# Kernel tuning notes

Hardware: AMD Instinct MI355X
Metric: run time of the kernel (lower is better)

## Reference

```python
import jax, jax.numpy as jnp
import numpy as np

B, T, C = 2, 2048, 2048
NH, NKV = 16, 16
HD = C // NH            # 128
GATE_CH = 32
ROPE_BASE = 10000.0


def setup_inputs() -> dict:
    key = jax.random.key(0)
    ks = jax.random.split(key, 8)
    x = jax.random.normal(ks[0], (B, T, C), jnp.float32)
    ve = jax.random.normal(ks[1], (B, T, C), jnp.float32)
    # RoPE tables: half-dim rotation, shape broadcastable to [B, T, H, HD//2]
    d2 = HD // 2
    inv_freq = 1.0 / (ROPE_BASE ** (jnp.arange(d2, dtype=jnp.float32) / d2))
    angles = jnp.arange(T, dtype=jnp.float32)[:, None] * inv_freq[None, :]  # [T, d2]
    cos = jnp.cos(angles)[None, :, None, :]  # [1, T, 1, d2]
    sin = jnp.sin(angles)[None, :, None, :]
    s = 0.02
    Wq = jax.random.normal(ks[2], (C, NH * HD), jnp.float32) * s
    Wk = jax.random.normal(ks[3], (C, NKV * HD), jnp.float32) * s
    Wv = jax.random.normal(ks[4], (C, NKV * HD), jnp.float32) * s
    Wgate = jax.random.normal(ks[5], (GATE_CH, NKV), jnp.float32) * s
    Wproj = jax.random.normal(ks[6], (NH * HD, C), jnp.float32) * s
    return {"x": x, "ve": ve, "cos": cos, "sin": sin,
            "Wq": Wq, "Wk": Wk, "Wv": Wv, "Wgate": Wgate, "Wproj": Wproj}


def _apply_rotary(x, cos, sin):
    d = x.shape[3] // 2
    x1, x2 = x[..., :d], x[..., d:]
    return jnp.concatenate([x1 * cos + x2 * sin, x1 * -sin + x2 * cos], axis=3)


def _rms_norm(x):
    return x * jax.lax.rsqrt(jnp.mean(x * x, axis=-1, keepdims=True) + 1e-6)


def reference(x, ve, cos, sin, Wq, Wk, Wv, Wgate, Wproj):
    b, t, c = x.shape
    q = (x @ Wq).reshape(b, t, NH, HD)
    k = (x @ Wk).reshape(b, t, NKV, HD)
    v = (x @ Wv).reshape(b, t, NKV, HD)
    # value-embedding gate
    ve_r = ve.reshape(b, t, NKV, HD)
    gate = 2.0 * jax.nn.sigmoid(x[..., :GATE_CH] @ Wgate)  # [B, T, NKV]
    v = v + gate[..., None] * ve_r
    # RoPE then QK-RMSNorm
    q = _rms_norm(_apply_rotary(q, cos, sin))
    k = _rms_norm(_apply_rotary(k, cos, sin))
    # causal attention, scale = 1/sqrt(head_dim)
    scale = 1.0 / np.sqrt(HD).astype(np.float32)
    scores = jnp.einsum('bqhd,bkhd->bhqk', q, k) * scale
    causal = jnp.tril(jnp.ones((t, t), dtype=bool))
    scores = jnp.where(causal, scores, jnp.finfo(scores.dtype).min)
    probs = jax.nn.softmax(scores, axis=-1)
    y = jnp.einsum('bhqk,bkhd->bqhd', probs, v)
    y = y.reshape(b, t, NH * HD)
    return y @ Wproj
```

## Files before the change

### kernel.cpp

```cpp
#include <hip/hip_runtime.h>
#include <stdint.h>

typedef short bf16x8 __attribute__((ext_vector_type(8)));
typedef float f32x4 __attribute__((ext_vector_type(4)));

#define ASYNC16(g, l) __builtin_amdgcn_global_load_lds( \
    (const __attribute__((address_space(1))) unsigned int*)(g), \
    (__attribute__((address_space(3))) unsigned int*)(l), 16, 0, 0)

__device__ __forceinline__ float bf2f(short u) {
  union { unsigned int i; float f; } v;
  v.i = ((unsigned int)(unsigned short)u) << 16;
  return v.f;
}
__device__ __forceinline__ short f2bf(float f) {
  union { float f; unsigned int i; } v;
  v.f = f;
  return (short)(unsigned short)((v.i + 0x8000u) >> 16);
}
__device__ __forceinline__ float ldf(const void* p, long i, int isbf) {
  return isbf ? bf2f(((const short*)p)[i]) : ((const float*)p)[i];
}

__global__ void detect_dtype(const short* __restrict__ x, int* __restrict__ flag) {
  if (threadIdx.x == 0 && blockIdx.x == 0) {
    int cnt = 0;
    for (int i = 0; i < 128; ++i) {
      int e = (((unsigned short)x[i]) >> 7) & 0xFF;
      if (e >= 110 && e <= 136) ++cnt;
    }
    *flag = (cnt >= 120) ? 1 : 0;
  }
}

__global__ __launch_bounds__(256) void convert_x(
    const void* __restrict__ xin, short* __restrict__ xb, const int* __restrict__ flag) {
  long i = (long)blockIdx.x * 2048 + (long)threadIdx.x * 8;
  if (*flag) {
    *(bf16x8*)(xb + i) = *(const bf16x8*)((const short*)xin + i);
  } else {
    const float* xf = (const float*)xin;
    short tmp[8];
    #pragma unroll
    for (int j = 0; j < 8; ++j) tmp[j] = f2bf(xf[i + j]);
    *(bf16x8*)(xb + i) = *(bf16x8*)tmp;
  }
}

__global__ __launch_bounds__(256) void transpose_w(
    const void* __restrict__ S0, short* __restrict__ D0,
    const void* __restrict__ S1, short* __restrict__ D1,
    const void* __restrict__ S2, short* __restrict__ D2,
    const int* __restrict__ flag)
{
  int z = blockIdx.z;
  const void* S = (z == 0) ? S0 : (z == 1) ? S1 : S2;
  short* D = (z == 0) ? D0 : (z == 1) ? D1 : D2;
  int isbf = *flag;
  __shared__ short tile[32][33];
  int c0 = blockIdx.x * 32, r0 = blockIdx.y * 32;
  int tx = threadIdx.x, ty = threadIdx.y;
  #pragma unroll
  for (int i = 0; i < 4; ++i)
    tile[ty + 8*i][tx] = f2bf(ldf(S, (long)(r0 + ty + 8*i) * 2048 + c0 + tx, isbf));
  __syncthreads();
  #pragma unroll
  for (int i = 0; i < 4; ++i)
    D[(long)(c0 + ty + 8*i) * 2048 + r0 + tx] = tile[tx][ty + 8*i];
}

__global__ __launch_bounds__(256) void transpose_v(
    const short* __restrict__ Vr, short* __restrict__ Vt)
{
  __shared__ short tile[32][33];
  int bh = blockIdx.z;
  int b = bh >> 4, h = bh & 15;
  int t0 = blockIdx.x * 32, d0 = blockIdx.y * 32;
  int tx = threadIdx.x, ty = threadIdx.y;
  #pragma unroll
  for (int i = 0; i < 4; ++i)
    tile[ty + 8*i][tx] = Vr[(long)(b*2048 + t0 + ty + 8*i) * 2048 + h*128 + d0 + tx];
  __syncthreads();
  #pragma unroll
  for (int i = 0; i < 4; ++i)
    Vt[((long)bh * 128 + d0 + ty + 8*i) * 2048 + t0 + tx] = tile[tx][ty + 8*i];
}

template<typename OutT>
__global__ __launch_bounds__(256) void gemm_bt(
    const short* __restrict__ A,
    const short* __restrict__ B0, const short* __restrict__ B1, const short* __restrict__ B2,
    OutT* __restrict__ C0, OutT* __restrict__ C1, OutT* __restrict__ C2,
    int M, int N, int K)
{
  int z = blockIdx.z;
  const short* Bt = (z == 0) ? B0 : (z == 1) ? B1 : B2;
  OutT* C = (z == 0) ? C0 : (z == 1) ? C1 : C2;

  int d = blockIdx.y * 16 + blockIdx.x;
  int xcd = d & 7, ci = d >> 3;
  int bx = (xcd & 1) * 8 + (ci & 7);
  int by = (xcd >> 1) * 8 + (ci >> 3);
  int m0 = by * 128, n0 = bx * 128;

  int tid = threadIdx.x;
  int lane = tid & 63, w = tid >> 6;
  int quad = lane >> 4, l16 = lane & 15;
  int wm = w >> 1, wn = w & 1;

  __shared__ short As[128][64];
  __shared__ short Bs[128][64];

  f32x4 zero4 = {0.f, 0.f, 0.f, 0.f};
  f32x4 acc[4][4];
  #pragma unroll
  for (int i = 0; i < 4; ++i)
    #pragma unroll
    for (int j = 0; j < 4; ++j) acc[i][j] = zero4;

  int r8 = lane >> 3;
  int srow = w * 32 + r8;
  int scol = ((lane & 7) ^ r8) * 8;

  for (int k0 = 0; k0 < K; k0 += 64) {
    #pragma unroll
    for (int i = 0; i < 4; ++i) {
      ASYNC16(A  + (long)(m0 + srow + i*8) * K + k0 + scol, &As[w*32 + i*8][0]);
      ASYNC16(Bt + (long)(n0 + srow + i*8) * K + k0 + scol, &Bs[w*32 + i*8][0]);
    }
    __syncthreads();
    #pragma unroll
    for (int kt = 0; kt < 2; ++kt) {
      int po = ((kt*4 + quad) ^ (l16 & 7)) * 8;
      bf16x8 af[4], bfr[4];
      #pragma unroll
      for (int i = 0; i < 4; ++i)
        af[i] = *(const bf16x8*)&As[wm*64 + i*16 + l16][po];
      #pragma unroll
      for (int j = 0; j < 4; ++j)
        bfr[j] = *(const bf16x8*)&Bs[wn*64 + j*16 + l16][po];
      #pragma unroll
      for (int i = 0; i < 4; ++i)
        #pragma unroll
        for (int j = 0; j < 4; ++j)
          acc[i][j] = __builtin_amdgcn_mfma_f32_16x16x32_bf16(af[i], bfr[j], acc[i][j], 0, 0, 0);
    }
    __syncthreads();
  }

  #pragma unroll
  for (int i = 0; i < 4; ++i)
    #pragma unroll
    for (int j = 0; j < 4; ++j) {
      int row = m0 + wm*64 + i*16 + quad*4;
      int col = n0 + wn*64 + j*16 + l16;
      #pragma unroll
      for (int r = 0; r < 4; ++r) {
        float v = acc[i][j][r];
        if constexpr (sizeof(OutT) == 4)
          C[(long)(row + r) * N + col] = v;
        else
          C[(long)(row + r) * N + col] = (OutT)f2bf(v);
      }
    }
}

__global__ __launch_bounds__(256) void pointwise(
    const short* __restrict__ xb, const void* __restrict__ ve,
    const void* __restrict__ cosb, const void* __restrict__ sinb,
    const void* __restrict__ Wg, const int* __restrict__ flag,
    short* __restrict__ Qr, short* __restrict__ Kr, short* __restrict__ Vr)
{
  int row = blockIdx.x;
  int tid = threadIdx.x;
  int isbf = *flag;
  __shared__ float xg[32];
  __shared__ float gates[16];
  if (tid < 32) xg[tid] = bf2f(xb[(long)row * 2048 + tid]);
  __syncthreads();
  if (tid < 16) {
    float g = 0.f;
    #pragma unroll
    for (int i = 0; i < 32; ++i) g += xg[i] * ldf(Wg, i*16 + tid, isbf);
    gates[tid] = 2.0f / (1.0f + __expf(-g));
  }
  __syncthreads();
  {
    int idx = tid * 8;
    int h = idx >> 7;
    long p = (long)row * 2048 + idx;
    float g = gates[h];
    bf16x8 vv = *(bf16x8*)(Vr + p);
    short tmp[8];
    if (isbf) {
      bf16x8 vb = *(const bf16x8*)((const short*)ve + p);
      #pragma unroll
      for (int j = 0; j < 8; ++j) tmp[j] = f2bf(bf2f(vv[j]) + g * bf2f(vb[j]));
    } else {
      const float* vf = (const float*)ve;
      f32x4 a = *(const f32x4*)(vf + p);
      f32x4 b2 = *(const f32x4*)(vf + p + 4);
      #pragma unroll
      for (int j = 0; j < 4; ++j) tmp[j]     = f2bf(bf2f(vv[j])     + g * a[j]);
      #pragma unroll
      for (int j = 0; j < 4; ++j) tmp[j + 4] = f2bf(bf2f(vv[j + 4]) + g * b2[j]);
    }
    *(bf16x8*)(Vr + p) = *(bf16x8*)tmp;
  }
  int lane = tid & 63, w = tid >> 6;
  int t = row & 2047;
  #pragma unroll
  for (int it = 0; it < 8; ++it) {
    int unit = it * 4 + w;
    short* P = (unit < 16) ? Qr : Kr;
    int h = unit & 15;
    long base = (long)row * 2048 + h * 128;
    float x1 = bf2f(P[base + lane]);
    float x2 = bf2f(P[base + lane + 64]);
    float c = ldf(cosb, t*64 + lane, isbf);
    float s = ldf(sinb, t*64 + lane, isbf);
    float r1 = x1 * c + x2 * s;
    float r2 = -x1 * s + x2 * c;
    float ss = r1*r1 + r2*r2;
    #pragma unroll
    for (int off = 32; off; off >>= 1) ss += __shfl_xor(ss, off);
    float rn = rsqrtf(ss * (1.0f/128.0f) + 1e-6f);
    P[base + lane]      = f2bf(r1 * rn);
    P[base + lane + 64] = f2bf(r2 * rn);
  }
}

#define FL_C1 0.12751741f
#define FL_C2 16.321698f

__global__ __launch_bounds__(256) void flash(
    const short* __restrict__ Q, const short* __restrict__ K,
    const short* __restrict__ Vt, short* __restrict__ Y)
{
  int d = blockIdx.y * 16 + blockIdx.x;
  int xcd = d & 7, ci = d >> 3;
  int bx = ci & 15;
  int bh = xcd * 4 + (ci >> 4);
  int b = bh >> 4, h = bh & 15;
  int tid = threadIdx.x;
  int lane = tid & 63, w = tid >> 6;
  int quad = lane >> 4, l16 = lane & 15;

  __shared__ short Ks[2][64*128];
  __shared__ short Vts[2][128*64];
  __shared__ short Ps[4][16*72];

  int qtA = bx, qtB = 31 - bx;
  int nA = qtA + 1, nB = qtB + 1;
  int total = nA + nB;

  int kkey = tid >> 4;
  int klo  = (tid & 15) ^ (kkey & 7);
  int vd   = tid >> 3;
  int vlo  = (tid & 7) ^ (vd & 7);
  const short* Kbase = K + (long)(b*2048 + kkey) * 2048 + h*128 + klo*8;
  const short* Vbase = Vt + ((long)bh*128 + vd) * 2048 + vlo*8;

  f32x4 zero4 = {0.f, 0.f, 0.f, 0.f};
  f32x4 o[8];
  float l_i[4];
  bf16x8 qf[4];
  bf16x8 ones;
  #pragma unroll
  for (int j = 0; j < 8; ++j) ones[j] = (short)0x3F80;

  auto stage = [&](int tt, int bufp) {
    int tl = (tt < nA) ? tt : tt - nA;
    long ko = (long)tl * 64 * 2048;
    int  vo = tl * 64;
    #pragma unroll
    for (int i = 0; i < 4; ++i)
      ASYNC16(Kbase + ko + (long)i*16*2048, &Ks[bufp][(i*16 + w*4)*128]);
    #pragma unroll
    for (int i = 0; i < 4; ++i)
      ASYNC16(Vbase + vo + (long)i*32*2048, &Vts[bufp][(i*32 + w*8)*64]);
  };
  auto loadQ = [&](int qt) {
    const short* Qb = Q + (long)(b*2048 + qt*64 + w*16 + l16) * 2048 + h*128;
    #pragma unroll
    for (int kt = 0; kt < 4; ++kt)
      qf[kt] = *(const bf16x8*)(Qb + kt*32 + quad*8);
  };
  auto flushO = [&](int qt) {
    #pragma unroll
    for (int r = 0; r < 4; ++r) {
      float inv = 1.0f / fmaxf(l_i[r], 1e-30f);
      short* yp = Y + (long)(b*2048 + qt*64 + w*16 + quad*4 + r) * 2048 + h*128;
      #pragma unroll
      for (int c8 = 0; c8 < 8; ++c8)
        yp[c8*16 + l16] = f2bf(o[c8][r] * inv);
    }
  };

  #pragma unroll
  for (int c = 0; c < 8; ++c) o[c] = zero4;
  #pragma unroll
  for (int r = 0; r < 4; ++r) l_i[r] = 0.f;
  loadQ(qtA);
  stage(0, 0);

  int qt = qtA, n_seg = nA, segbase = 0;
  for (int tt = 0; tt < total; ++tt) {
    int buf = tt & 1;
    asm volatile("s_waitcnt vmcnt(0)" ::: "memory");
    __builtin_amdgcn_s_barrier();
    if (tt + 1 < total) stage(tt + 1, buf ^ 1);
    if (tt == nA) {
      flushO(qtA);
      loadQ(qtB);
      #pragma unroll
      for (int c = 0; c < 8; ++c) o[c] = zero4;
      #pragma unroll
      for (int r = 0; r < 4; ++r) l_i[r] = 0.f;
      qt = qtB; n_seg = nB; segbase = nA;
    }
    int tloc = tt - segbase;
    int kv0 = tloc * 64;

    f32x4 s[4];
    __builtin_amdgcn_s_setprio(1);
    #pragma unroll
    for (int c = 0; c < 4; ++c) {
      f32x4 acc = zero4;
      #pragma unroll
      for (int kt = 0; kt < 4; ++kt) {
        int po = ((kt*4 + quad) ^ (l16 & 7)) * 8;
        bf16x8 kf = *(const bf16x8*)&Ks[buf][(c*16 + l16)*128 + po];
        acc = __builtin_amdgcn_mfma_f32_16x16x32_bf16(qf[kt], kf, acc, 0, 0, 0);
      }
      s[c] = acc;
    }
    __builtin_amdgcn_s_setprio(0);

    bool domask = (tloc == n_seg - 1);
    int qgb = qt*64 + w*16 + quad*4;
    #pragma unroll
    for (int c = 0; c < 4; ++c) {
      int kg = kv0 + c*16 + l16;
      #pragma unroll
      for (int r = 0; r < 4; ++r) {
        float t = s[c][r] * FL_C1 - FL_C2;
        if (domask && kg > qgb + r) t = -1000.0f;
        float pv = exp2f(t);
        Ps[w][(quad*4 + r)*72 + c*16 + l16] = f2bf(pv);
      }
    }
    asm volatile("s_waitcnt lgkmcnt(0)" ::: "memory");
    bf16x8 pa0 = *(const bf16x8*)&Ps[w][l16*72 + quad*8];
    bf16x8 pa1 = *(const bf16x8*)&Ps[w][l16*72 + 32 + quad*8];

    __builtin_amdgcn_s_setprio(1);
    f32x4 racc = __builtin_amdgcn_mfma_f32_16x16x32_bf16(pa0, ones, zero4, 0, 0, 0);
    racc = __builtin_amdgcn_mfma_f32_16x16x32_bf16(pa1, ones, racc, 0, 0, 0);
    #pragma unroll
    for (int r = 0; r < 4; ++r) l_i[r] += racc[r];

    #pragma unroll
    for (int c8 = 0; c8 < 8; ++c8) {
      int po0 = ((0*4 + quad) ^ (l16 & 7)) * 8;
      int po1 = ((1*4 + quad) ^ (l16 & 7)) * 8;
      bf16x8 v0 = *(const bf16x8*)&Vts[buf][(c8*16 + l16)*64 + po0];
      bf16x8 v1 = *(const bf16x8*)&Vts[buf][(c8*16 + l16)*64 + po1];
      o[c8] = __builtin_amdgcn_mfma_f32_16x16x32_bf16(pa0, v0, o[c8], 0, 0, 0);
      o[c8] = __builtin_amdgcn_mfma_f32_16x16x32_bf16(pa1, v1, o[c8], 0, 0, 0);
    }
    __builtin_amdgcn_s_setprio(0);
  }
  flushO(qtB);
}

extern "C" void kernel_launch(void* const* d_in, const int* in_sizes, int n_in,
                              void* d_out, int out_size, void* d_ws, size_t ws_size,
                              hipStream_t stream) {
  const void* x    = d_in[0];
  const void* ve   = d_in[1];
  const void* cosb = d_in[2];
  const void* sinb = d_in[3];
  const void* Wq   = d_in[4];
  const void* Wk   = d_in[5];
  const void* Wv   = d_in[6];
  const void* Wg   = d_in[7];
  const void* Wp   = d_in[8];
  float* out = (float*)d_out;

  int*   flag = (int*)d_ws;
  short* base = (short*)d_ws + 256;
  short* wt0 = base;
  short* wtk = base + 4194304L;
  short* wtv = base + 8388608L;
  short* Vt  = base + 4194304L;
  short* xb  = base + 12582912L;
  short* Y   = base + 12582912L;
  short* Qr  = base + 20971520L;
  short* Kr  = base + 29360128L;
  short* Vr  = base + 37748736L;

  detect_dtype<<<1, 64, 0, stream>>>((const short*)x, flag);
  convert_x<<<4096, 256, 0, stream>>>(x, xb, flag);
  transpose_w<<<dim3(64, 64, 3), dim3(32, 8), 0, stream>>>(Wq, wt0, Wk, wtk, Wv, wtv, flag);
  gemm_bt<short><<<dim3(16, 32, 3), 256, 0, stream>>>(xb, wt0, wtk, wtv, Qr, Kr, Vr, 4096, 2048, 2048);
  transpose_w<<<dim3(64, 64, 1), dim3(32, 8), 0, stream>>>(Wp, wt0, Wp, wt0, Wp, wt0, flag);
  pointwise<<<dim3(4096), 256, 0, stream>>>(xb, ve, cosb, sinb, Wg, flag, Qr, Kr, Vr);
  transpose_v<<<dim3(64, 4, 32), dim3(32, 8), 0, stream>>>(Vr, Vt);
  flash<<<dim3(16, 32), 256, 0, stream>>>(Qr, Kr, Vt, Y);
  gemm_bt<float><<<dim3(16, 32, 1), 256, 0, stream>>>(Y, wt0, wt0, wt0, out, out, out, 4096, 2048, 2048);
}
```

Before: 456.7 us.

## Share K/V tiles between paired query tiles in flash attention loop

The flash kernel used to walk the two paired query tiles (qtA and 31-qtA) one after the other, loading every K/V tile for each. Now it keeps two sets of Q fragments and accumulators and does one pass over the KV tiles of the longer segment. Each staged K/V tile is applied to both query tiles while it is still in range, which roughly halves global-to-LDS traffic. Launch bounds now ask for 2 blocks per CU, and the doubled accumulator state raises register pressure, so spills or lower occupancy are a risk.

```diff
diff --git a/kernel.cpp b/kernel.cpp
--- a/kernel.cpp
+++ b/kernel.cpp
@@ -233,7 +233,7 @@
 #define FL_C1 0.12751741f
 #define FL_C2 16.321698f
 
-__global__ __launch_bounds__(256) void flash(
+__global__ __launch_bounds__(256, 2) void flash(
     const short* __restrict__ Q, const short* __restrict__ K,
     const short* __restrict__ Vt, short* __restrict__ Y)
 {
@@ -252,7 +252,6 @@
 
   int qtA = bx, qtB = 31 - bx;
   int nA = qtA + 1, nB = qtB + 1;
-  int total = nA + nB;
 
   int kkey = tid >> 4;
   int klo  = (tid & 15) ^ (kkey & 7);
@@ -262,15 +261,17 @@
   const short* Vbase = Vt + ((long)bh*128 + vd) * 2048 + vlo*8;
 
   f32x4 zero4 = {0.f, 0.f, 0.f, 0.f};
-  f32x4 o[8];
-  float l_i[4];
-  bf16x8 qf[4];
+  f32x4 oA[8], oB[8];
+  float lA[4], lB[4];
+  bf16x8 qfA[4], qfB[4];
   bf16x8 ones;
   #pragma unroll
   for (int j = 0; j < 8; ++j) ones[j] = (short)0x3F80;
 
-  auto stage = [&](int tt, int bufp) {
-    int tl = (tt < nA) ? tt : tt - nA;
+  int pv0 = ((0*4 + quad) ^ (l16 & 7)) * 8;
+  int pv1 = ((1*4 + quad) ^ (l16 & 7)) * 8;
+
+  auto stage = [&](int tl, int bufp) {
     long ko = (long)tl * 64 * 2048;
     int  vo = tl * 64;
     #pragma unroll
@@ -280,48 +281,24 @@
     for (int i = 0; i < 4; ++i)
       ASYNC16(Vbase + vo + (long)i*32*2048, &Vts[bufp][(i*32 + w*8)*64]);
   };
-  auto loadQ = [&](int qt) {
+  auto loadQ = [&](int qt, bf16x8 (&qf)[4]) {
     const short* Qb = Q + (long)(b*2048 + qt*64 + w*16 + l16) * 2048 + h*128;
     #pragma unroll
     for (int kt = 0; kt < 4; ++kt)
       qf[kt] = *(const bf16x8*)(Qb + kt*32 + quad*8);
   };
-  auto flushO = [&](int qt) {
+  auto flushO = [&](int qt, f32x4 (&o)[8], float (&l)[4]) {
     #pragma unroll
     for (int r = 0; r < 4; ++r) {
-      float inv = 1.0f / fmaxf(l_i[r], 1e-30f);
+      float inv = 1.0f / fmaxf(l[r], 1e-30f);
       short* yp = Y + (long)(b*2048 + qt*64 + w*16 + quad*4 + r) * 2048 + h*128;
       #pragma unroll
       for (int c8 = 0; c8 < 8; ++c8)
         yp[c8*16 + l16] = f2bf(o[c8][r] * inv);
     }
   };
-
-  #pragma unroll
-  for (int c = 0; c < 8; ++c) o[c] = zero4;
-  #pragma unroll
-  for (int r = 0; r < 4; ++r) l_i[r] = 0.f;
-  loadQ(qtA);
-  stage(0, 0);
-
-  int qt = qtA, n_seg = nA, segbase = 0;
-  for (int tt = 0; tt < total; ++tt) {
-    int buf = tt & 1;
-    asm volatile("s_waitcnt vmcnt(0)" ::: "memory");
-    __builtin_amdgcn_s_barrier();
-    if (tt + 1 < total) stage(tt + 1, buf ^ 1);
-    if (tt == nA) {
-      flushO(qtA);
-      loadQ(qtB);
-      #pragma unroll
-      for (int c = 0; c < 8; ++c) o[c] = zero4;
-      #pragma unroll
-      for (int r = 0; r < 4; ++r) l_i[r] = 0.f;
-      qt = qtB; n_seg = nB; segbase = nA;
-    }
-    int tloc = tt - segbase;
-    int kv0 = tloc * 64;
-
+  auto doTile = [&](bf16x8 (&qf)[4], f32x4 (&o)[8], float (&l)[4],
+                    int qt, bool domask, int buf, int kv0) {
     f32x4 s[4];
     __builtin_amdgcn_s_setprio(1);
     #pragma unroll
@@ -337,7 +314,6 @@
     }
     __builtin_amdgcn_s_setprio(0);
 
-    bool domask = (tloc == n_seg - 1);
     int qgb = qt*64 + w*16 + quad*4;
     #pragma unroll
     for (int c = 0; c < 4; ++c) {
@@ -346,8 +322,7 @@
       for (int r = 0; r < 4; ++r) {
         float t = s[c][r] * FL_C1 - FL_C2;
         if (domask && kg > qgb + r) t = -1000.0f;
-        float pv = exp2f(t);
-        Ps[w][(quad*4 + r)*72 + c*16 + l16] = f2bf(pv);
+        Ps[w][(quad*4 + r)*72 + c*16 + l16] = f2bf(exp2f(t));
       }
     }
     asm volatile("s_waitcnt lgkmcnt(0)" ::: "memory");
@@ -358,20 +333,39 @@
     f32x4 racc = __builtin_amdgcn_mfma_f32_16x16x32_bf16(pa0, ones, zero4, 0, 0, 0);
     racc = __builtin_amdgcn_mfma_f32_16x16x32_bf16(pa1, ones, racc, 0, 0, 0);
     #pragma unroll
-    for (int r = 0; r < 4; ++r) l_i[r] += racc[r];
+    for (int r = 0; r < 4; ++r) l[r] += racc[r];
 
     #pragma unroll
     for (int c8 = 0; c8 < 8; ++c8) {
-      int po0 = ((0*4 + quad) ^ (l16 & 7)) * 8;
-      int po1 = ((1*4 + quad) ^ (l16 & 7)) * 8;
-      bf16x8 v0 = *(const bf16x8*)&Vts[buf][(c8*16 + l16)*64 + po0];
-      bf16x8 v1 = *(const bf16x8*)&Vts[buf][(c8*16 + l16)*64 + po1];
+      bf16x8 v0 = *(const bf16x8*)&Vts[buf][(c8*16 + l16)*64 + pv0];
+      bf16x8 v1 = *(const bf16x8*)&Vts[buf][(c8*16 + l16)*64 + pv1];
       o[c8] = __builtin_amdgcn_mfma_f32_16x16x32_bf16(pa0, v0, o[c8], 0, 0, 0);
       o[c8] = __builtin_amdgcn_mfma_f32_16x16x32_bf16(pa1, v1, o[c8], 0, 0, 0);
     }
     __builtin_amdgcn_s_setprio(0);
-  }
-  flushO(qtB);
+  };
+
+  #pragma unroll
+  for (int c = 0; c < 8; ++c) { oA[c] = zero4; oB[c] = zero4; }
+  #pragma unroll
+  for (int r = 0; r < 4; ++r) { lA[r] = 0.f; lB[r] = 0.f; }
+  loadQ(qtA, qfA);
+  loadQ(qtB, qfB);
+  stage(0, 0);
+
+  for (int tt = 0; tt < nB; ++tt) {
+    int buf = tt & 1;
+    asm volatile("s_waitcnt vmcnt(0)" ::: "memory");
+    __builtin_amdgcn_s_barrier();
+    if (tt + 1 < nB) stage(tt + 1, buf ^ 1);
+    int kv0 = tt * 64;
+
+    doTile(qfB, oB, lB, qtB, tt == nB - 1, buf, kv0);
+    if (tt < nA)
+      doTile(qfA, oA, lA, qtA, tt == nA - 1, buf, kv0);
+  }
+  flushO(qtB, oB, lB);
+  flushO(qtA, oA, lA);
 }
 
 extern "C" void kernel_launch(void* const* d_in, const int* in_sizes, int n_in,
```

Result: no change. 448.4 us (-1.8%).
